# Kernel tuning notes

Hardware: AMD Instinct MI355X
Metric: run time of the kernel (lower is better)

## Reference

```python
import jax, jax.numpy as jnp
import numpy as np

LOG2E = 1.4426950408889634  # 1/ln(2): kernel works in log2 space with exp2


def _mlstm_chunkwise_single(q, k, v, vecI, vecF, chunk_size):
    # q,k: [T,K]; v: [T,V]; vecI,vecF: [T] (log2-space gate preactivations)
    T, K = q.shape
    V = v.shape[-1]
    BT = chunk_size
    NT = T // BT
    scale = K ** -0.5
    dt = q.dtype

    qc = q.reshape(NT, BT, K)
    kc = k.reshape(NT, BT, K)
    vc = v.reshape(NT, BT, V)
    ic = vecI.reshape(NT, BT)
    fc = vecF.reshape(NT, BT)
    b = jnp.cumsum(fc, axis=1)            # within-chunk cumulative log2 forget (vecF in kernel)
    f_last = b[:, -1]                      # scaF_last
    g = ic + f_last[:, None] - b           # decay from each pos to chunk end (vecG)

    tri = jnp.tril(jnp.ones((BT, BT), dtype=bool))

    def step(carry, inp):
        C, n, m = carry                    # [K,V], [K], scalar running max
        qt, kt, vt, it, bt, gt, fl = inp
        # intra-chunk decay matrix D[t,s] = i[s] + b[t] - b[s] for s<=t
        D = it[None, :] + bt[:, None] - bt[None, :]
        D = jnp.where(tri, D, -jnp.inf)
        m_intra = jnp.max(D, axis=1)                      # [BT]
        m_total = jnp.maximum(bt + m, m_intra)            # matM_total
        S = (qt @ kt.T) * (scale * jnp.exp2(D - m_total[:, None]))
        q_sc = qt * (scale * jnp.exp2(bt + m - m_total))[:, None]
        h_num = q_sc @ C + S @ vt                          # [BT,V]
        denom = jnp.maximum(jnp.abs(q_sc @ n + S.sum(axis=1)), jnp.exp2(-m_total))
        h = h_num / denom[:, None]
        # cross-chunk matrix-state recurrence with log2 restabilization
        m_next = jnp.maximum(fl + m, jnp.max(gt))
        dec = jnp.exp2(fl + m - m_next)
        kdec = kt * jnp.exp2(gt - m_next)[:, None]         # [BT,K]
        C_next = C * dec + kdec.T @ vt
        n_next = n * dec + kdec.sum(axis=0)
        return (C_next, n_next, m_next), h

    C0 = jnp.zeros((K, V), dt)
    n0 = jnp.zeros((K,), dt)
    m0 = jnp.zeros((), dt)
    _, hs = jax.lax.scan(step, (C0, n0, m0), (qc, kc, vc, ic, b, g, f_last))
    return hs.reshape(T, V)


def setup_inputs() -> dict:
    key = jax.random.key(0)
    ks = jax.random.split(key, 5)
    B, H, T, D = 8, 8, 4096, 64
    q = jax.random.normal(ks[0], (B, H, T, D), dtype=jnp.float32)
    k = jax.random.normal(ks[1], (B, H, T, D), dtype=jnp.float32)
    v = jax.random.normal(ks[2], (B, H, T, D), dtype=jnp.float32)
    i = jax.random.normal(ks[3], (B, H, T), dtype=jnp.float32)
    f = jax.random.normal(ks[4], (B, H, T), dtype=jnp.float32)
    return {"q": q, "k": k, "v": v, "i": i, "f": f, "chunk_size": 64}


def reference(q, k, v, i, f, chunk_size):
    B, H, T, K = q.shape
    V = v.shape[-1]
    vecF = jax.nn.log_sigmoid(f) * LOG2E   # log2 sigmoid(f)
    vecI = i * LOG2E                       # input gate in log2 space
    BH = B * H
    fn = lambda qq, kk, vv, ii, ff: _mlstm_chunkwise_single(qq, kk, vv, ii, ff, chunk_size)
    h = jax.vmap(fn)(q.reshape(BH, T, K), k.reshape(BH, T, K), v.reshape(BH, T, V),
                     vecI.reshape(BH, T), vecF.reshape(BH, T))
    return h.reshape(B, H, T, V)
```

## Files before the change

kernel.cpp:

```cpp
#include <hip/hip_runtime.h>
#include <hip/hip_bf16.h>
#include <math.h>

#define LOG2E_F 1.4426950408889634f

static constexpr int BT = 64;
static constexpr int DK = 64;
static constexpr int DV = 64;
static constexpr float SCALE = 0.125f;
static constexpr int PAD = 72;

typedef unsigned short ushort_t;
typedef __attribute__((ext_vector_type(8))) short short8;
typedef __attribute__((ext_vector_type(4))) float f32x4;
typedef __attribute__((ext_vector_type(4))) ushort_t ushort4v;

#define MFMA16(a, b, c) __builtin_amdgcn_mfma_f32_16x16x32_bf16((a), (b), (c), 0, 0, 0)

__device__ __forceinline__ int SWZ(int a, int b){ return a * PAD + (b ^ (((a >> 3) & 3) << 3)); }
__device__ __forceinline__ int ZSW(int r, int c){ return r * PAD + (c ^ (((r >> 2) & 3) << 3)); }
__device__ __forceinline__ int LIN(int r, int c){ return r * PAD + c; }

__device__ __forceinline__ float logsig_log2e(float x){
    float l = (x >= 0.f) ? (-log1pf(expf(-x))) : (x - log1pf(expf(x)));
    return l * LOG2E_F;
}
__device__ __forceinline__ ushort_t f2bf(float x){
    unsigned u = __builtin_bit_cast(unsigned, x);
    unsigned r = u + 0x7FFFu + ((u >> 16) & 1u);
    return (ushort_t)(r >> 16);
}
__device__ __forceinline__ float bf2f(ushort_t u){
    return __builtin_bit_cast(float, ((unsigned)u) << 16);
}
__device__ __forceinline__ void split_bf(float x, ushort_t& h, ushort_t& l){
    h = f2bf(x);
    l = f2bf(x - bf2f(h));
}

__global__ __launch_bounds__(256, 4) void stageA_kernel(
    const float* __restrict__ kg, const float* __restrict__ vg,
    const float* __restrict__ ig, const float* __restrict__ fg,
    float* __restrict__ A_ws, float* __restrict__ nloc_ws,
    float* __restrict__ fl_ws, float* __restrict__ mloc_ws,
    int T, int NT)
{
    const int ct = blockIdx.x, s = blockIdx.y, tid = threadIdx.x;
    const int w = tid >> 6, lane = tid & 63, ln = lane & 15, quad = lane >> 4;
    const int q8 = quad * 8;

    __shared__ __align__(16) ushort_t kth[BT * PAD];
    __shared__ __align__(16) ushort_t ktl[BT * PAD];
    __shared__ __align__(16) ushort_t vth[BT * PAD];
    __shared__ __align__(16) ushort_t vtl[BT * PAD];
    __shared__ float gsc[BT];

    const size_t rowbase = (size_t)s * T + (size_t)ct * BT;
    const float* kc = kg + rowbase * DK;
    const float* vc = vg + rowbase * DV;

    float4 kr[4], vr[4];
    #pragma unroll
    for (int i = 0; i < 4; ++i){
        int idx = i * 1024 + tid * 4;
        kr[i] = *(const float4*)(kc + idx);
        vr[i] = *(const float4*)(vc + idx);
    }
    if (tid < 64){
        float b = logsig_log2e(fg[rowbase + tid]);
        #pragma unroll
        for (int off = 1; off < 64; off <<= 1){
            float y = __shfl_up(b, off);
            if (tid >= off) b += y;
        }
        float f_last = __shfl(b, 63);
        float a = ig[rowbase + tid] * LOG2E_F - b;
        float p = a;
        #pragma unroll
        for (int off = 32; off > 0; off >>= 1) p = fmaxf(p, __shfl_xor(p, off));
        gsc[tid] = exp2f(a - p);
        if (tid == 0){ fl_ws[s * NT + ct] = f_last; mloc_ws[s * NT + ct] = f_last + p; }
    }
    __syncthreads();
    #pragma unroll
    for (int i = 0; i < 4; ++i){
        int idx = i * 1024 + tid * 4;
        int r = idx >> 6, c0 = idx & 63;
        float g = gsc[r];
        float kv[4] = {kr[i].x * g, kr[i].y * g, kr[i].z * g, kr[i].w * g};
        float vv[4] = {vr[i].x, vr[i].y, vr[i].z, vr[i].w};
        #pragma unroll
        for (int j = 0; j < 4; ++j){
            ushort_t h, l;
            split_bf(kv[j], h, l); kth[SWZ(c0 + j, r)] = h; ktl[SWZ(c0 + j, r)] = l;
            split_bf(vv[j], h, l); vth[SWZ(c0 + j, r)] = h; vtl[SWZ(c0 + j, r)] = l;
        }
    }
    __syncthreads();

    const int m = 16 * w + ln;
    short8 ah0 = *(const short8*)&kth[SWZ(m, q8)];
    short8 ah1 = *(const short8*)&kth[SWZ(m, 32 + q8)];
    short8 al0 = *(const short8*)&ktl[SWZ(m, q8)];
    short8 al1 = *(const short8*)&ktl[SWZ(m, 32 + q8)];
    float* Ab = A_ws + (size_t)(s * NT + ct) * 4096;
    #pragma unroll
    for (int t = 0; t < 4; ++t){
        f32x4 acc = {0.f, 0.f, 0.f, 0.f};
        short8 bh0 = *(const short8*)&vth[SWZ(16 * t + ln, q8)];
        short8 bh1 = *(const short8*)&vth[SWZ(16 * t + ln, 32 + q8)];
        short8 bl0 = *(const short8*)&vtl[SWZ(16 * t + ln, q8)];
        short8 bl1 = *(const short8*)&vtl[SWZ(16 * t + ln, 32 + q8)];
        acc = MFMA16(ah0, bh0, acc);
        acc = MFMA16(ah1, bh1, acc);
        acc = MFMA16(ah0, bl0, acc);
        acc = MFMA16(ah1, bl1, acc);
        acc = MFMA16(al0, bh0, acc);
        acc = MFMA16(al1, bh1, acc);
        *(f32x4*)(Ab + ((16 * t + ln) << 6) + 16 * w + quad * 4) = acc;
    }
    {
        short8 ones;
        #pragma unroll
        for (int j = 0; j < 8; ++j) ones[j] = (short)0x3F80;
        f32x4 nacc = {0.f, 0.f, 0.f, 0.f};
        nacc = MFMA16(ah0, ones, nacc);
        nacc = MFMA16(ah1, ones, nacc);
        nacc = MFMA16(al0, ones, nacc);
        nacc = MFMA16(al1, ones, nacc);
        if (ln == 0){
            #pragma unroll
            for (int reg = 0; reg < 4; ++reg)
                nloc_ws[((size_t)(s * NT + ct)) * DK + 16 * w + quad * 4 + reg] = nacc[reg];
        }
    }
}

__global__ __launch_bounds__(256) void stageB_kernel(
    const float* __restrict__ A_ws, const float* __restrict__ nloc_ws,
    const float* __restrict__ fl_ws, const float* __restrict__ mloc_ws,
    float* __restrict__ Cws, float* __restrict__ nws, float* __restrict__ mws,
    int NT)
{
    const int vb = blockIdx.x, s = blockIdx.y, tid = threadIdx.x;
    __shared__ float decs[64], scs[64];

    if (tid < 64){
        float fl = fl_ws[s * NT + tid];
        float ml = mloc_ws[s * NT + tid];
        float F = fl, G = ml;
        #pragma unroll
        for (int off = 1; off < 64; off <<= 1){
            float Fp = __shfl_up(F, off);
            float Gp = __shfl_up(G, off);
            if (tid >= off){ G = fmaxf(Gp + F, G); F = Fp + F; }
        }
        float m_next = fmaxf(F, G);
        float m_cur  = __shfl_up(m_next, 1);
        if (tid == 0) m_cur = 0.f;
        decs[tid] = exp2f(fl + m_cur - m_next);
        scs[tid]  = exp2f(ml - m_next);
        if (vb == 0) mws[s * NT + tid] = m_cur;
    }
    __syncthreads();

    const size_t base = (size_t)s * NT * 4096 + (size_t)vb * 256 + tid;
    const float* Ab = A_ws + base;
    float*       Cb = Cws  + base;
    const bool do_n = (vb == 0) && (tid < 64);

    float C = 0.f, nreg = 0.f;
    float p[8], nl[8];
    #pragma unroll
    for (int i = 0; i < 8; ++i){ p[i] = Ab[(size_t)i * 4096]; nl[i] = 0.f; }
    if (do_n){
        #pragma unroll
        for (int i = 0; i < 8; ++i) nl[i] = nloc_ws[((size_t)(s * NT + i)) * DK + tid];
    }

    for (int t0 = 0; t0 < NT; t0 += 8){
        float qv[8], nq[8];
        const int tn = t0 + 8;
        #pragma unroll
        for (int i = 0; i < 8; ++i)
            qv[i] = (tn + i < NT) ? Ab[(size_t)(tn + i) * 4096] : 0.f;
        #pragma unroll
        for (int i = 0; i < 8; ++i) nq[i] = 0.f;
        if (do_n){
            #pragma unroll
            for (int i = 0; i < 8; ++i)
                if (tn + i < NT) nq[i] = nloc_ws[((size_t)(s * NT + tn + i)) * DK + tid];
        }
        #pragma unroll
        for (int i = 0; i < 8; ++i){
            const int t = t0 + i;
            Cb[(size_t)t * 4096] = C;
            if (do_n) nws[((size_t)(s * NT + t)) * DK + tid] = nreg;
            const float d = decs[t], sc = scs[t];
            C = C * d + p[i] * sc;
            if (do_n) nreg = nreg * d + nl[i] * sc;
        }
        #pragma unroll
        for (int i = 0; i < 8; ++i){ p[i] = qv[i]; nl[i] = nq[i]; }
    }
}

__global__ __launch_bounds__(256, 4) void pass2_kernel(
    const float* __restrict__ qg, const float* __restrict__ kg, const float* __restrict__ vg,
    const float* __restrict__ ig, const float* __restrict__ fg,
    const float* __restrict__ Cws, const float* __restrict__ nws, const float* __restrict__ mws,
    float* __restrict__ out, int T, int NT)
{
    const int ct = blockIdx.x, s = blockIdx.y, tid = threadIdx.x;
    const int w = tid >> 6, lane = tid & 63, ln = lane & 15, quad = lane >> 4;
    const int q8 = quad * 8;

    __shared__ __align__(16) ushort_t bufA[BT * PAD];
    __shared__ __align__(16) ushort_t bufB[BT * PAD];
    __shared__ __align__(16) ushort_t bufZ[BT * PAD];
    __shared__ __align__(16) ushort_t bufV[BT * PAD];
    __shared__ float colterm[BT], Mr[BT], rowfac[BT], dncl[BT];
    __shared__ float nsh[DK], qn[BT], rowsum[BT];

    const size_t rowbase = (size_t)s * T + (size_t)ct * BT;
    const float* qc = qg + rowbase * DK;
    const float* kc = kg + rowbase * DK;
    const float* vc = vg + rowbase * DV;
    const float* Cc = Cws + ((size_t)(s * NT + ct)) * 4096;
    const float* nc = nws + ((size_t)(s * NT + ct)) * DK;
    const float m   = mws[s * NT + ct];

    float4 kr4[4], vr[4];
    #pragma unroll
    for (int i = 0; i < 4; ++i){
        int idx = i * 1024 + tid * 4;
        kr4[i] = *(const float4*)(kc + idx);
        vr[i]  = *(const float4*)(vc + idx);
    }
    const float* qrow = qc + (16 * w + ln) * DK;
    float4 qf0 = *(const float4*)(qrow + q8);
    float4 qf1 = *(const float4*)(qrow + q8 + 4);
    float4 qf2 = *(const float4*)(qrow + 32 + q8);
    float4 qf3 = *(const float4*)(qrow + 32 + q8 + 4);
    float4 Cr[4];
    #pragma unroll
    for (int i = 0; i < 4; ++i)
        Cr[i] = *(const float4*)(Cc + i * 1024 + tid * 4);

    if (tid < 64){
        float b = logsig_log2e(fg[rowbase + tid]);
        #pragma unroll
        for (int off = 1; off < 64; off <<= 1){
            float y = __shfl_up(b, off);
            if (tid >= off) b += y;
        }
        float a = ig[rowbase + tid] * LOG2E_F - b;
        float p = a;
        #pragma unroll
        for (int off = 1; off < 64; off <<= 1){
            float y = __shfl_up(p, off);
            if (tid >= off) p = fmaxf(p, y);
        }
        float M = fmaxf(m, p);
        colterm[tid] = a;
        Mr[tid] = M;
        rowfac[tid] = SCALE * exp2f(m - M);
        dncl[tid] = exp2f(-(b + M));
        nsh[tid] = nc[tid];
    }
    #pragma unroll
    for (int i = 0; i < 4; ++i){
        int idx = i * 1024 + tid * 4;
        int r = idx >> 6, c0 = idx & 63;
        float kv[4] = {kr4[i].x, kr4[i].y, kr4[i].z, kr4[i].w};
        ushort4v kh4, kl4;
        #pragma unroll
        for (int j = 0; j < 4; ++j){
            ushort_t h, l;
            split_bf(kv[j], h, l); kh4[j] = h; kl4[j] = l;
        }
        *(ushort4v*)&bufA[SWZ(r, c0)] = kh4;
        *(ushort4v*)&bufB[SWZ(r, c0)] = kl4;
    }
    __syncthreads();

    const int mrow = 16 * w + ln;
    float a0[8] = {qf0.x, qf0.y, qf0.z, qf0.w, qf1.x, qf1.y, qf1.z, qf1.w};
    float a1[8] = {qf2.x, qf2.y, qf2.z, qf2.w, qf3.x, qf3.y, qf3.z, qf3.w};
    short8 ah0, al0, ah1, al1;
    #pragma unroll
    for (int j = 0; j < 8; ++j){
        ushort_t h, l;
        split_bf(a0[j], h, l); ah0[j] = (short)h; al0[j] = (short)l;
        split_bf(a1[j], h, l); ah1[j] = (short)h; al1[j] = (short)l;
    }
    {
        float p = 0.f;
        #pragma unroll
        for (int j = 0; j < 8; ++j){
            p = fmaf(a0[j], nsh[q8 + j], p);
            p = fmaf(a1[j], nsh[32 + q8 + j], p);
        }
        p += __shfl_xor(p, 16);
        p += __shfl_xor(p, 32);
        if (quad == 0) qn[mrow] = p;
    }
    #pragma unroll
    for (int i = 0; i < 4; ++i){
        int idx = i * 1024 + tid * 4;
        int r = idx >> 6, c0 = idx & 63;
        float vv[4] = {vr[i].x, vr[i].y, vr[i].z, vr[i].w};
        #pragma unroll
        for (int j = 0; j < 4; ++j) bufV[SWZ(c0 + j, r)] = f2bf(vv[j]);
    }

    f32x4 sacc[4];
    #pragma unroll
    for (int t = 0; t < 4; ++t){
        sacc[t] = (f32x4){0.f, 0.f, 0.f, 0.f};
        short8 bh0 = *(const short8*)&bufA[SWZ(16 * t + ln, q8)];
        short8 bh1 = *(const short8*)&bufA[SWZ(16 * t + ln, 32 + q8)];
        short8 bl0 = *(const short8*)&bufB[SWZ(16 * t + ln, q8)];
        short8 bl1 = *(const short8*)&bufB[SWZ(16 * t + ln, 32 + q8)];
        sacc[t] = MFMA16(ah0, bh0, sacc[t]);
        sacc[t] = MFMA16(ah1, bh1, sacc[t]);
        sacc[t] = MFMA16(ah0, bl0, sacc[t]);
        sacc[t] = MFMA16(ah1, bl1, sacc[t]);
        sacc[t] = MFMA16(al0, bh0, sacc[t]);
        sacc[t] = MFMA16(al1, bh1, sacc[t]);
    }
    {
        float rsum[4] = {0.f, 0.f, 0.f, 0.f};
        float Mrv[4];
        #pragma unroll
        for (int reg = 0; reg < 4; ++reg) Mrv[reg] = Mr[16 * w + quad * 4 + reg];
        #pragma unroll
        for (int t = 0; t < 4; ++t){
            int c = 16 * t + ln;
            float cterm = colterm[c];
            #pragma unroll
            for (int reg = 0; reg < 4; ++reg){
                int r = 16 * w + quad * 4 + reg;
                float vS = (c <= r) ? sacc[t][reg] * SCALE * exp2f(cterm - Mrv[reg]) : 0.f;
                bufZ[ZSW(r, c)] = f2bf(vS);
                rsum[reg] += vS;
            }
        }
        #pragma unroll
        for (int off = 1; off < 16; off <<= 1){
            #pragma unroll
            for (int reg = 0; reg < 4; ++reg) rsum[reg] += __shfl_xor(rsum[reg], off);
        }
        if (ln == 0){
            #pragma unroll
            for (int reg = 0; reg < 4; ++reg) rowsum[16 * w + quad * 4 + reg] = rsum[reg];
        }
    }
    __syncthreads();

    #pragma unroll
    for (int i = 0; i < 4; ++i){
        int idx = i * 1024 + tid * 4;
        int vrow = idx >> 6, k0 = idx & 63;
        float cv[4] = {Cr[i].x, Cr[i].y, Cr[i].z, Cr[i].w};
        ushort4v ch4, cl4;
        #pragma unroll
        for (int j = 0; j < 4; ++j){
            ushort_t h, l;
            split_bf(cv[j], h, l); ch4[j] = h; cl4[j] = l;
        }
        *(ushort4v*)&bufA[SWZ(vrow, k0)] = ch4;
        *(ushort4v*)&bufB[SWZ(vrow, k0)] = cl4;
    }
    __syncthreads();

    f32x4 acc[4];
    #pragma unroll
    for (int t = 0; t < 4; ++t){
        acc[t] = (f32x4){0.f, 0.f, 0.f, 0.f};
        short8 bh0 = *(const short8*)&bufA[SWZ(16 * t + ln, q8)];
        short8 bh1 = *(const short8*)&bufA[SWZ(16 * t + ln, 32 + q8)];
        short8 bl0 = *(const short8*)&bufB[SWZ(16 * t + ln, q8)];
        short8 bl1 = *(const short8*)&bufB[SWZ(16 * t + ln, 32 + q8)];
        acc[t] = MFMA16(ah0, bh0, acc[t]);
        acc[t] = MFMA16(ah1, bh1, acc[t]);
        acc[t] = MFMA16(ah0, bl0, acc[t]);
        acc[t] = MFMA16(ah1, bl1, acc[t]);
        acc[t] = MFMA16(al0, bh0, acc[t]);
        acc[t] = MFMA16(al1, bh1, acc[t]);
    }
    float rf[4], inv[4];
    #pragma unroll
    for (int reg = 0; reg < 4; ++reg){
        int r = 16 * w + quad * 4 + reg;
        rf[reg] = rowfac[r];
        float dn = fabsf(rf[reg] * qn[r] + rowsum[r]);
        inv[reg] = 1.f / fmaxf(dn, dncl[r]);
    }
    #pragma unroll
    for (int t = 0; t < 4; ++t){
        #pragma unroll
        for (int reg = 0; reg < 4; ++reg) acc[t][reg] *= rf[reg];
    }
    short8 az0 = *(const short8*)&bufZ[ZSW(mrow, q8)];
    short8 az1 = *(const short8*)&bufZ[ZSW(mrow, 32 + q8)];
    #pragma unroll
    for (int t = 0; t < 4; ++t){
        short8 bh0 = *(const short8*)&bufV[SWZ(16 * t + ln, q8)];
        short8 bh1 = *(const short8*)&bufV[SWZ(16 * t + ln, 32 + q8)];
        acc[t] = MFMA16(az0, bh0, acc[t]);
        acc[t] = MFMA16(az1, bh1, acc[t]);
    }
    #pragma unroll
    for (int t = 0; t < 4; ++t){
        int c = 16 * t + ln;
        #pragma unroll
        for (int reg = 0; reg < 4; ++reg){
            int r = 16 * w + quad * 4 + reg;
            out[(rowbase + r) * DV + c] = acc[t][reg] * inv[reg];
        }
    }
}

__global__ __launch_bounds__(256) void fused_kernel(
    const float* __restrict__ qg, const float* __restrict__ kg, const float* __restrict__ vg,
    const float* __restrict__ ig, const float* __restrict__ fg,
    float* __restrict__ out, int T, int NT)
{
    const int s = blockIdx.x;
    const int tid = threadIdx.x;
    const int lane = tid & 63;

    __shared__ float X[BT][DK + 1];
    __shared__ float Y[BT][DK + 1];
    __shared__ float Cb[DK][DV];
    __shared__ __hip_bfloat16 Zh[BT][BT];
    __shared__ float colterm[BT], Mr[BT], rowfac[BT], dncl[BT], gscale[BT];
    __shared__ float nsh[DK], qn[BT], rowsum[BT], denom[BT];
    __shared__ float sh_dec;

    const float* qseq = qg + (size_t)s * T * DK;
    const float* kseq = kg + (size_t)s * T * DK;
    const float* vseq = vg + (size_t)s * T * DV;
    const float* iseq = ig + (size_t)s * T;
    const float* fseq = fg + (size_t)s * T;

    for (int idx = tid; idx < DK * DV; idx += 256) Cb[idx >> 6][idx & 63] = 0.f;
    if (tid < 64) nsh[lane] = 0.f;
    float m = 0.f;
    __syncthreads();

    const int r0 = (tid >> 4) * 4;
    const int c0 = (tid & 15) * 4;
    const int v0 = c0;

    for (int t = 0; t < NT; ++t){
        const size_t rb = (size_t)t * BT;
        if (tid < 64){
            float b = logsig_log2e(fseq[rb + lane]);
            #pragma unroll
            for (int off = 1; off < 64; off <<= 1){
                float y = __shfl_up(b, off);
                if (lane >= off) b += y;
            }
            float f_last = __shfl(b, 63);
            float a = iseq[rb + lane] * LOG2E_F - b;
            float p = a;
            #pragma unroll
            for (int off = 1; off < 64; off <<= 1){
                float y = __shfl_up(p, off);
                if (lane >= off) p = fmaxf(p, y);
            }
            float M = fmaxf(m, p);
            colterm[lane] = a;
            Mr[lane] = M;
            rowfac[lane] = SCALE * exp2f(m - M);
            dncl[lane] = exp2f(-(b + M));
            float g = a + f_last;
            float gm = g;
            #pragma unroll
            for (int off = 32; off > 0; off >>= 1) gm = fmaxf(gm, __shfl_xor(gm, off));
            float m_next = fmaxf(f_last + m, gm);
            gscale[lane] = exp2f(g - m_next);
            if (tid == 0) sh_dec = exp2f(f_last + m - m_next);
            m = m_next;
        }
        #pragma unroll
        for (int base = 0; base < BT * DK; base += 1024){
            int idx = base + tid * 4;
            int r = idx >> 6, c = idx & 63;
            float4 a4 = *(const float4*)(qseq + rb * DK + idx);
            X[r][c] = a4.x; X[r][c+1] = a4.y; X[r][c+2] = a4.z; X[r][c+3] = a4.w;
            float4 b4 = *(const float4*)(kseq + rb * DK + idx);
            Y[r][c] = b4.x; Y[r][c+1] = b4.y; Y[r][c+2] = b4.z; Y[r][c+3] = b4.w;
        }
        __syncthreads();

        float sacc[4][4] = {};
        for (int x = 0; x < DK; ++x){
            float xr[4], yc[4];
            #pragma unroll
            for (int j = 0; j < 4; ++j) xr[j] = X[r0 + j][x];
            #pragma unroll
            for (int j = 0; j < 4; ++j) yc[j] = Y[c0 + j][x];
            #pragma unroll
            for (int j = 0; j < 4; ++j)
                #pragma unroll
                for (int jj = 0; jj < 4; ++jj)
                    sacc[j][jj] = fmaf(xr[j], yc[jj], sacc[j][jj]);
        }
        float rs[4];
        #pragma unroll
        for (int j = 0; j < 4; ++j){
            int r = r0 + j;
            float Mrv = Mr[r];
            float acc = 0.f;
            #pragma unroll
            for (int jj = 0; jj < 4; ++jj){
                int c = c0 + jj;
                float vS = (c <= r) ? sacc[j][jj] * SCALE * exp2f(colterm[c] - Mrv) : 0.f;
                Zh[r][c] = __float2bfloat16(vS);
                acc += vS;
            }
            rs[j] = acc;
        }
        #pragma unroll
        for (int off = 1; off < 16; off <<= 1){
            #pragma unroll
            for (int j = 0; j < 4; ++j) rs[j] += __shfl_xor(rs[j], off);
        }
        if ((tid & 15) == 0){
            #pragma unroll
            for (int j = 0; j < 4; ++j) rowsum[r0 + j] = rs[j];
        }
        float acc1[4][4] = {};
        for (int x = 0; x < DK; ++x){
            float xr[4], yv[4];
            #pragma unroll
            for (int j = 0; j < 4; ++j) xr[j] = X[r0 + j][x];
            #pragma unroll
            for (int j = 0; j < 4; ++j) yv[j] = Cb[x][v0 + j];
            #pragma unroll
            for (int j = 0; j < 4; ++j)
                #pragma unroll
                for (int jj = 0; jj < 4; ++jj)
                    acc1[j][jj] = fmaf(xr[j], yv[jj], acc1[j][jj]);
        }
        if (tid < 64){
            float acc = 0.f;
            for (int x = 0; x < DK; ++x) acc = fmaf(X[lane][x], nsh[x], acc);
            qn[lane] = acc;
        }
        __syncthreads();

        #pragma unroll
        for (int base = 0; base < BT * DV; base += 1024){
            int idx = base + tid * 4;
            int r = idx >> 6, c = idx & 63;
            float4 a4 = *(const float4*)(vseq + rb * DV + idx);
            X[r][c] = a4.x; X[r][c+1] = a4.y; X[r][c+2] = a4.z; X[r][c+3] = a4.w;
        }
        if (tid < 64){
            float dn = fabsf(rowfac[lane] * qn[lane] + rowsum[lane]);
            denom[lane] = fmaxf(dn, dncl[lane]);
        }
        __syncthreads();

        float acc2[4][4] = {};
        for (int c = 0; c < BT; ++c){
            float zr[4], xv[4];
            #pragma unroll
            for (int j = 0; j < 4; ++j) zr[j] = __bfloat162float(Zh[r0 + j][c]);
            #pragma unroll
            for (int j = 0; j < 4; ++j) xv[j] = X[c][v0 + j];
            #pragma unroll
            for (int j = 0; j < 4; ++j)
                #pragma unroll
                for (int jj = 0; jj < 4; ++jj)
                    acc2[j][jj] = fmaf(zr[j], xv[jj], acc2[j][jj]);
        }
        #pragma unroll
        for (int j = 0; j < 4; ++j){
            int r = r0 + j;
            float rf = rowfac[r];
            float inv = 1.f / denom[r];
            float4 h4;
            h4.x = (acc1[j][0] * rf + acc2[j][0]) * inv;
            h4.y = (acc1[j][1] * rf + acc2[j][1]) * inv;
            h4.z = (acc1[j][2] * rf + acc2[j][2]) * inv;
            h4.w = (acc1[j][3] * rf + acc2[j][3]) * inv;
            *(float4*)(out + ((size_t)s * T + rb + r) * DV + v0) = h4;
        }
        {
            float dec = sh_dec;
            float cr[4][4];
            #pragma unroll
            for (int j = 0; j < 4; ++j)
                #pragma unroll
                for (int jj = 0; jj < 4; ++jj)
                    cr[j][jj] = Cb[r0 + j][c0 + jj] * dec;
            for (int c = 0; c < BT; ++c){
                float gs = gscale[c];
                float kd[4], xv[4];
                #pragma unroll
                for (int j = 0; j < 4; ++j) kd[j] = Y[c][r0 + j] * gs;
                #pragma unroll
                for (int jj = 0; jj < 4; ++jj) xv[jj] = X[c][c0 + jj];
                #pragma unroll
                for (int j = 0; j < 4; ++j)
                    #pragma unroll
                    for (int jj = 0; jj < 4; ++jj)
                        cr[j][jj] = fmaf(kd[j], xv[jj], cr[j][jj]);
            }
            #pragma unroll
            for (int j = 0; j < 4; ++j)
                #pragma unroll
                for (int jj = 0; jj < 4; ++jj)
                    Cb[r0 + j][c0 + jj] = cr[j][jj];
        }
        if (tid < 64){
            float acc = 0.f;
            for (int c = 0; c < BT; ++c) acc = fmaf(Y[c][lane], gscale[c], acc);
            nsh[lane] = nsh[lane] * sh_dec + acc;
        }
        __syncthreads();
    }
}

extern "C" void kernel_launch(void* const* d_in, const int* in_sizes, int n_in,
                              void* d_out, int out_size, void* d_ws, size_t ws_size,
                              hipStream_t stream)
{
    const float* q  = (const float*)d_in[0];
    const float* k  = (const float*)d_in[1];
    const float* v  = (const float*)d_in[2];
    const float* ii = (const float*)d_in[3];
    const float* ff = (const float*)d_in[4];
    float* out = (float*)d_out;

    const int T  = 4096;
    const int BH = in_sizes[3] / T;
    const int NT = T / BT;

    const size_t szC  = (size_t)BH * NT * DK * DV * sizeof(float);
    const size_t szA  = szC;
    const size_t szn  = (size_t)BH * NT * DK * sizeof(float);
    const size_t szs  = (size_t)BH * NT * sizeof(float);

    const size_t need_new = szA + szC + 2 * szn + 3 * szs;

    if (ws_size >= need_new){
        char* p = (char*)d_ws;
        float* A_ws    = (float*)p;            p += szA;
        float* Cws     = (float*)p;            p += szC;
        float* nloc_ws = (float*)p;            p += szn;
        float* nws     = (float*)p;            p += szn;
        float* fl_ws   = (float*)p;            p += szs;
        float* mloc_ws = (float*)p;            p += szs;
        float* mws     = (float*)p;
        stageA_kernel<<<dim3(NT, BH), 256, 0, stream>>>(k, v, ii, ff, A_ws, nloc_ws, fl_ws, mloc_ws, T, NT);
        stageB_kernel<<<dim3(16, BH), 256, 0, stream>>>(A_ws, nloc_ws, fl_ws, mloc_ws, Cws, nws, mws, NT);
        pass2_kernel<<<dim3(NT, BH), 256, 0, stream>>>(q, k, v, ii, ff, Cws, nws, mws, out, T, NT);
    } else {
        fused_kernel<<<dim3(BH), 256, 0, stream>>>(q, k, v, ii, ff, out, T, NT);
    }
}
```

Measured before the change: 292.1 us.

## Checkpoint chunk states every four chunks and recompute intermediates in pass2

StageB now writes the inter-chunk C/n state only at every fourth chunk, plus per-chunk decay and scale factors. Pass2 processes four consecutive chunks per block and rebuilds the running state in registers from the checkpoint and the per-chunk A contributions. This cuts the write and re-read of the full per-chunk C state workspace. In exchange it reads A_ws again, launches four times fewer pass2 blocks with a serial loop inside each, and recombines q from its split bf16 halves, which slightly changes rounding.

```diff
diff --git a/kernel.cpp b/kernel.cpp
--- a/kernel.cpp
+++ b/kernel.cpp
@@ -9,6 +9,7 @@
 static constexpr int DV = 64;
 static constexpr float SCALE = 0.125f;
 static constexpr int PAD = 72;
+static constexpr int CPB = 4;
 
 typedef unsigned short ushort_t;
 typedef __attribute__((ext_vector_type(8))) short short8;
@@ -19,7 +20,6 @@
 
 __device__ __forceinline__ int SWZ(int a, int b){ return a * PAD + (b ^ (((a >> 3) & 3) << 3)); }
 __device__ __forceinline__ int ZSW(int r, int c){ return r * PAD + (c ^ (((r >> 2) & 3) << 3)); }
-__device__ __forceinline__ int LIN(int r, int c){ return r * PAD + c; }
 
 __device__ __forceinline__ float logsig_log2e(float x){
     float l = (x >= 0.f) ? (-log1pf(expf(-x))) : (x - log1pf(expf(x)));
@@ -139,10 +139,12 @@
 __global__ __launch_bounds__(256) void stageB_kernel(
     const float* __restrict__ A_ws, const float* __restrict__ nloc_ws,
     const float* __restrict__ fl_ws, const float* __restrict__ mloc_ws,
-    float* __restrict__ Cws, float* __restrict__ nws, float* __restrict__ mws,
+    float* __restrict__ Cb_ws, float* __restrict__ nb_ws,
+    float* __restrict__ mws, float* __restrict__ decs_ws, float* __restrict__ scs_ws,
     int NT)
 {
     const int vb = blockIdx.x, s = blockIdx.y, tid = threadIdx.x;
+    const int NG = NT >> 2;
     __shared__ float decs[64], scs[64];
 
     if (tid < 64){
@@ -158,15 +160,20 @@
         float m_next = fmaxf(F, G);
         float m_cur  = __shfl_up(m_next, 1);
         if (tid == 0) m_cur = 0.f;
-        decs[tid] = exp2f(fl + m_cur - m_next);
-        scs[tid]  = exp2f(ml - m_next);
-        if (vb == 0) mws[s * NT + tid] = m_cur;
+        float d  = exp2f(fl + m_cur - m_next);
+        float sc = exp2f(ml - m_next);
+        decs[tid] = d;
+        scs[tid]  = sc;
+        if (vb == 0){
+            mws[s * NT + tid]     = m_cur;
+            decs_ws[s * NT + tid] = d;
+            scs_ws[s * NT + tid]  = sc;
+        }
     }
     __syncthreads();
 
     const size_t base = (size_t)s * NT * 4096 + (size_t)vb * 256 + tid;
     const float* Ab = A_ws + base;
-    float*       Cb = Cws  + base;
     const bool do_n = (vb == 0) && (tid < 64);
 
     float C = 0.f, nreg = 0.f;
@@ -194,8 +201,11 @@
         #pragma unroll
         for (int i = 0; i < 8; ++i){
             const int t = t0 + i;
-            Cb[(size_t)t * 4096] = C;
-            if (do_n) nws[((size_t)(s * NT + t)) * DK + tid] = nreg;
+            if ((t & 3) == 0){
+                const int g = t >> 2;
+                Cb_ws[((size_t)(s * NG + g)) * 4096 + (size_t)vb * 256 + tid] = C;
+                if (do_n) nb_ws[((size_t)(s * NG + g)) * 64 + tid] = nreg;
+            }
             const float d = decs[t], sc = scs[t];
             C = C * d + p[i] * sc;
             if (do_n) nreg = nreg * d + nl[i] * sc;
@@ -208,12 +218,17 @@
 __global__ __launch_bounds__(256, 4) void pass2_kernel(
     const float* __restrict__ qg, const float* __restrict__ kg, const float* __restrict__ vg,
     const float* __restrict__ ig, const float* __restrict__ fg,
-    const float* __restrict__ Cws, const float* __restrict__ nws, const float* __restrict__ mws,
+    const float* __restrict__ A_ws, const float* __restrict__ Cb_ws,
+    const float* __restrict__ nb_ws, const float* __restrict__ nloc_ws,
+    const float* __restrict__ mws, const float* __restrict__ decs_ws,
+    const float* __restrict__ scs_ws,
     float* __restrict__ out, int T, int NT)
 {
-    const int ct = blockIdx.x, s = blockIdx.y, tid = threadIdx.x;
+    const int g = blockIdx.x, s = blockIdx.y, tid = threadIdx.x;
     const int w = tid >> 6, lane = tid & 63, ln = lane & 15, quad = lane >> 4;
     const int q8 = quad * 8;
+    const int ct0 = g * CPB;
+    const int NG = NT >> 2;
 
     __shared__ __align__(16) ushort_t bufA[BT * PAD];
     __shared__ __align__(16) ushort_t bufB[BT * PAD];
@@ -222,203 +237,239 @@
     __shared__ float colterm[BT], Mr[BT], rowfac[BT], dncl[BT];
     __shared__ float nsh[DK], qn[BT], rowsum[BT];
 
-    const size_t rowbase = (size_t)s * T + (size_t)ct * BT;
-    const float* qc = qg + rowbase * DK;
-    const float* kc = kg + rowbase * DK;
-    const float* vc = vg + rowbase * DV;
-    const float* Cc = Cws + ((size_t)(s * NT + ct)) * 4096;
-    const float* nc = nws + ((size_t)(s * NT + ct)) * DK;
-    const float m   = mws[s * NT + ct];
-
-    float4 kr4[4], vr[4];
+    f32x4 Crun[4];
+    {
+        const float* Cb = Cb_ws + ((size_t)(s * NG + g)) * 4096;
+        #pragma unroll
+        for (int i = 0; i < 4; ++i)
+            Crun[i] = *(const f32x4*)(Cb + i * 1024 + tid * 4);
+    }
+    if (tid < 64) nsh[tid] = nb_ws[((size_t)(s * NG + g)) * 64 + tid];
+
+    float fvs[CPB], ivs[CPB], nlv[CPB], mvs[CPB], dcv[CPB], scv[CPB];
     #pragma unroll
-    for (int i = 0; i < 4; ++i){
-        int idx = i * 1024 + tid * 4;
-        kr4[i] = *(const float4*)(kc + idx);
-        vr[i]  = *(const float4*)(vc + idx);
-    }
-    const float* qrow = qc + (16 * w + ln) * DK;
-    float4 qf0 = *(const float4*)(qrow + q8);
-    float4 qf1 = *(const float4*)(qrow + q8 + 4);
-    float4 qf2 = *(const float4*)(qrow + 32 + q8);
-    float4 qf3 = *(const float4*)(qrow + 32 + q8 + 4);
-    float4 Cr[4];
+    for (int c = 0; c < CPB; ++c){
+        const int ct = ct0 + c;
+        const size_t rb = (size_t)s * T + (size_t)ct * BT;
+        fvs[c] = 0.f; ivs[c] = 0.f; nlv[c] = 0.f;
+        if (tid < 64){
+            fvs[c] = fg[rb + tid];
+            ivs[c] = ig[rb + tid];
+            nlv[c] = nloc_ws[((size_t)(s * NT + ct)) * DK + tid];
+        }
+        mvs[c] = mws[s * NT + ct];
+        dcv[c] = decs_ws[s * NT + ct];
+        scv[c] = scs_ws[s * NT + ct];
+    }
+
     #pragma unroll
-    for (int i = 0; i < 4; ++i)
-        Cr[i] = *(const float4*)(Cc + i * 1024 + tid * 4);
-
-    if (tid < 64){
-        float b = logsig_log2e(fg[rowbase + tid]);
-        #pragma unroll
-        for (int off = 1; off < 64; off <<= 1){
-            float y = __shfl_up(b, off);
-            if (tid >= off) b += y;
-        }
-        float a = ig[rowbase + tid] * LOG2E_F - b;
-        float p = a;
-        #pragma unroll
-        for (int off = 1; off < 64; off <<= 1){
-            float y = __shfl_up(p, off);
-            if (tid >= off) p = fmaxf(p, y);
-        }
-        float M = fmaxf(m, p);
-        colterm[tid] = a;
-        Mr[tid] = M;
-        rowfac[tid] = SCALE * exp2f(m - M);
-        dncl[tid] = exp2f(-(b + M));
-        nsh[tid] = nc[tid];
-    }
-    #pragma unroll
-    for (int i = 0; i < 4; ++i){
-        int idx = i * 1024 + tid * 4;
-        int r = idx >> 6, c0 = idx & 63;
-        float kv[4] = {kr4[i].x, kr4[i].y, kr4[i].z, kr4[i].w};
-        ushort4v kh4, kl4;
-        #pragma unroll
-        for (int j = 0; j < 4; ++j){
-            ushort_t h, l;
-            split_bf(kv[j], h, l); kh4[j] = h; kl4[j] = l;
-        }
-        *(ushort4v*)&bufA[SWZ(r, c0)] = kh4;
-        *(ushort4v*)&bufB[SWZ(r, c0)] = kl4;
-    }
-    __syncthreads();
-
-    const int mrow = 16 * w + ln;
-    float a0[8] = {qf0.x, qf0.y, qf0.z, qf0.w, qf1.x, qf1.y, qf1.z, qf1.w};
-    float a1[8] = {qf2.x, qf2.y, qf2.z, qf2.w, qf3.x, qf3.y, qf3.z, qf3.w};
-    short8 ah0, al0, ah1, al1;
-    #pragma unroll
-    for (int j = 0; j < 8; ++j){
-        ushort_t h, l;
-        split_bf(a0[j], h, l); ah0[j] = (short)h; al0[j] = (short)l;
-        split_bf(a1[j], h, l); ah1[j] = (short)h; al1[j] = (short)l;
-    }
-    {
-        float p = 0.f;
-        #pragma unroll
-        for (int j = 0; j < 8; ++j){
-            p = fmaf(a0[j], nsh[q8 + j], p);
-            p = fmaf(a1[j], nsh[32 + q8 + j], p);
-        }
-        p += __shfl_xor(p, 16);
-        p += __shfl_xor(p, 32);
-        if (quad == 0) qn[mrow] = p;
-    }
-    #pragma unroll
-    for (int i = 0; i < 4; ++i){
-        int idx = i * 1024 + tid * 4;
-        int r = idx >> 6, c0 = idx & 63;
-        float vv[4] = {vr[i].x, vr[i].y, vr[i].z, vr[i].w};
-        #pragma unroll
-        for (int j = 0; j < 4; ++j) bufV[SWZ(c0 + j, r)] = f2bf(vv[j]);
-    }
-
-    f32x4 sacc[4];
-    #pragma unroll
-    for (int t = 0; t < 4; ++t){
-        sacc[t] = (f32x4){0.f, 0.f, 0.f, 0.f};
-        short8 bh0 = *(const short8*)&bufA[SWZ(16 * t + ln, q8)];
-        short8 bh1 = *(const short8*)&bufA[SWZ(16 * t + ln, 32 + q8)];
-        short8 bl0 = *(const short8*)&bufB[SWZ(16 * t + ln, q8)];
-        short8 bl1 = *(const short8*)&bufB[SWZ(16 * t + ln, 32 + q8)];
-        sacc[t] = MFMA16(ah0, bh0, sacc[t]);
-        sacc[t] = MFMA16(ah1, bh1, sacc[t]);
-        sacc[t] = MFMA16(ah0, bl0, sacc[t]);
-        sacc[t] = MFMA16(ah1, bl1, sacc[t]);
-        sacc[t] = MFMA16(al0, bh0, sacc[t]);
-        sacc[t] = MFMA16(al1, bh1, sacc[t]);
-    }
-    {
-        float rsum[4] = {0.f, 0.f, 0.f, 0.f};
-        float Mrv[4];
-        #pragma unroll
-        for (int reg = 0; reg < 4; ++reg) Mrv[reg] = Mr[16 * w + quad * 4 + reg];
+    for (int c = 0; c < CPB; ++c){
+        const int ct = ct0 + c;
+        const size_t rowbase = (size_t)s * T + (size_t)ct * BT;
+
+        float4 kr4[4], vr[4], qf[4];
+        #pragma unroll
+        for (int i = 0; i < 4; ++i){
+            int idx = i * 1024 + tid * 4;
+            kr4[i] = *(const float4*)(kg + rowbase * DK + idx);
+            vr[i]  = *(const float4*)(vg + rowbase * DV + idx);
+        }
+        {
+            const float* qrow = qg + (rowbase + 16 * w + ln) * DK;
+            qf[0] = *(const float4*)(qrow + q8);
+            qf[1] = *(const float4*)(qrow + q8 + 4);
+            qf[2] = *(const float4*)(qrow + 32 + q8);
+            qf[3] = *(const float4*)(qrow + 32 + q8 + 4);
+        }
+        if (tid < 64){
+            float b = logsig_log2e(fvs[c]);
+            #pragma unroll
+            for (int off = 1; off < 64; off <<= 1){
+                float y = __shfl_up(b, off);
+                if (tid >= off) b += y;
+            }
+            float a = ivs[c] * LOG2E_F - b;
+            float p = a;
+            #pragma unroll
+            for (int off = 1; off < 64; off <<= 1){
+                float y = __shfl_up(p, off);
+                if (tid >= off) p = fmaxf(p, y);
+            }
+            float M = fmaxf(mvs[c], p);
+            colterm[tid] = a;
+            Mr[tid] = M;
+            rowfac[tid] = SCALE * exp2f(mvs[c] - M);
+            dncl[tid] = exp2f(-(b + M));
+        }
+        #pragma unroll
+        for (int i = 0; i < 4; ++i){
+            int idx = i * 1024 + tid * 4;
+            int r = idx >> 6, c0 = idx & 63;
+            float kv[4] = {kr4[i].x, kr4[i].y, kr4[i].z, kr4[i].w};
+            ushort4v kh4, kl4;
+            #pragma unroll
+            for (int j = 0; j < 4; ++j){
+                ushort_t h, l;
+                split_bf(kv[j], h, l); kh4[j] = h; kl4[j] = l;
+            }
+            *(ushort4v*)&bufA[SWZ(r, c0)] = kh4;
+            *(ushort4v*)&bufB[SWZ(r, c0)] = kl4;
+        }
+        short8 ah0, al0, ah1, al1;
+        {
+            float a0t[8] = {qf[0].x, qf[0].y, qf[0].z, qf[0].w, qf[1].x, qf[1].y, qf[1].z, qf[1].w};
+            float a1t[8] = {qf[2].x, qf[2].y, qf[2].z, qf[2].w, qf[3].x, qf[3].y, qf[3].z, qf[3].w};
+            #pragma unroll
+            for (int j = 0; j < 8; ++j){
+                ushort_t h, l;
+                split_bf(a0t[j], h, l); ah0[j] = (short)h; al0[j] = (short)l;
+                split_bf(a1t[j], h, l); ah1[j] = (short)h; al1[j] = (short)l;
+            }
+        }
+        f32x4 Ar[4];
+        if (c + 1 < CPB){
+            const float* Ab = A_ws + ((size_t)(s * NT + ct)) * 4096;
+            #pragma unroll
+            for (int i = 0; i < 4; ++i)
+                Ar[i] = *(const f32x4*)(Ab + i * 1024 + tid * 4);
+        }
+        __syncthreads();
+
+        const int mrow = 16 * w + ln;
+        {
+            float p = 0.f;
+            #pragma unroll
+            for (int j = 0; j < 8; ++j){
+                float qv0 = bf2f((ushort_t)ah0[j]) + bf2f((ushort_t)al0[j]);
+                float qv1 = bf2f((ushort_t)ah1[j]) + bf2f((ushort_t)al1[j]);
+                p = fmaf(qv0, nsh[q8 + j], p);
+                p = fmaf(qv1, nsh[32 + q8 + j], p);
+            }
+            p += __shfl_xor(p, 16);
+            p += __shfl_xor(p, 32);
+            if (quad == 0) qn[mrow] = p;
+        }
+        #pragma unroll
+        for (int i = 0; i < 4; ++i){
+            int idx = i * 1024 + tid * 4;
+            int r = idx >> 6, c0 = idx & 63;
+            float vv[4] = {vr[i].x, vr[i].y, vr[i].z, vr[i].w};
+            #pragma unroll
+            for (int j = 0; j < 4; ++j) bufV[SWZ(c0 + j, r)] = f2bf(vv[j]);
+        }
+        f32x4 sacc[4];
         #pragma unroll
         for (int t = 0; t < 4; ++t){
-            int c = 16 * t + ln;
-            float cterm = colterm[c];
+            sacc[t] = (f32x4){0.f, 0.f, 0.f, 0.f};
+            short8 bh0 = *(const short8*)&bufA[SWZ(16 * t + ln, q8)];
+            short8 bh1 = *(const short8*)&bufA[SWZ(16 * t + ln, 32 + q8)];
+            short8 bl0 = *(const short8*)&bufB[SWZ(16 * t + ln, q8)];
+            short8 bl1 = *(const short8*)&bufB[SWZ(16 * t + ln, 32 + q8)];
+            sacc[t] = MFMA16(ah0, bh0, sacc[t]);
+            sacc[t] = MFMA16(ah1, bh1, sacc[t]);
+            sacc[t] = MFMA16(ah0, bl0, sacc[t]);
+            sacc[t] = MFMA16(ah1, bl1, sacc[t]);
+            sacc[t] = MFMA16(al0, bh0, sacc[t]);
+            sacc[t] = MFMA16(al1, bh1, sacc[t]);
+        }
+        {
+            float rsum[4] = {0.f, 0.f, 0.f, 0.f};
+            float Mrv[4];
+            #pragma unroll
+            for (int reg = 0; reg < 4; ++reg) Mrv[reg] = Mr[16 * w + quad * 4 + reg];
+            #pragma unroll
+            for (int t = 0; t < 4; ++t){
+                int cc = 16 * t + ln;
+                float cterm = colterm[cc];
+                #pragma unroll
+                for (int reg = 0; reg < 4; ++reg){
+                    int r = 16 * w + quad * 4 + reg;
+                    float vS = (cc <= r) ? sacc[t][reg] * SCALE * exp2f(cterm - Mrv[reg]) : 0.f;
+                    bufZ[ZSW(r, cc)] = f2bf(vS);
+                    rsum[reg] += vS;
+                }
+            }
+            #pragma unroll
+            for (int off = 1; off < 16; off <<= 1){
+                #pragma unroll
+                for (int reg = 0; reg < 4; ++reg) rsum[reg] += __shfl_xor(rsum[reg], off);
+            }
+            if (ln == 0){
+                #pragma unroll
+                for (int reg = 0; reg < 4; ++reg) rowsum[16 * w + quad * 4 + reg] = rsum[reg];
+            }
+        }
+        __syncthreads();
+
+        #pragma unroll
+        for (int i = 0; i < 4; ++i){
+            int idx = i * 1024 + tid * 4;
+            int vrow = idx >> 6, k0 = idx & 63;
+            float cv[4] = {Crun[i][0], Crun[i][1], Crun[i][2], Crun[i][3]};
+            ushort4v ch4, cl4;
+            #pragma unroll
+            for (int j = 0; j < 4; ++j){
+                ushort_t h, l;
+                split_bf(cv[j], h, l); ch4[j] = h; cl4[j] = l;
+            }
+            *(ushort4v*)&bufA[SWZ(vrow, k0)] = ch4;
+            *(ushort4v*)&bufB[SWZ(vrow, k0)] = cl4;
+        }
+        if (c + 1 < CPB){
+            #pragma unroll
+            for (int i = 0; i < 4; ++i)
+                Crun[i] = Crun[i] * dcv[c] + Ar[i] * scv[c];
+            if (tid < 64) nsh[tid] = nsh[tid] * dcv[c] + nlv[c] * scv[c];
+        }
+        __syncthreads();
+
+        f32x4 acc[4];
+        #pragma unroll
+        for (int t = 0; t < 4; ++t){
+            acc[t] = (f32x4){0.f, 0.f, 0.f, 0.f};
+            short8 bh0 = *(const short8*)&bufA[SWZ(16 * t + ln, q8)];
+            short8 bh1 = *(const short8*)&bufA[SWZ(16 * t + ln, 32 + q8)];
+            short8 bl0 = *(const short8*)&bufB[SWZ(16 * t + ln, q8)];
+            short8 bl1 = *(const short8*)&bufB[SWZ(16 * t + ln, 32 + q8)];
+            acc[t] = MFMA16(ah0, bh0, acc[t]);
+            acc[t] = MFMA16(ah1, bh1, acc[t]);
+            acc[t] = MFMA16(ah0, bl0, acc[t]);
+            acc[t] = MFMA16(ah1, bl1, acc[t]);
+            acc[t] = MFMA16(al0, bh0, acc[t]);
+            acc[t] = MFMA16(al1, bh1, acc[t]);
+        }
+        float rf[4], inv[4];
+        #pragma unroll
+        for (int reg = 0; reg < 4; ++reg){
+            int r = 16 * w + quad * 4 + reg;
+            rf[reg] = rowfac[r];
+            float dn = fabsf(rf[reg] * qn[r] + rowsum[r]);
+            inv[reg] = 1.f / fmaxf(dn, dncl[r]);
+        }
+        #pragma unroll
+        for (int t = 0; t < 4; ++t){
+            #pragma unroll
+            for (int reg = 0; reg < 4; ++reg) acc[t][reg] *= rf[reg];
+        }
+        short8 az0 = *(const short8*)&bufZ[ZSW(mrow, q8)];
+        short8 az1 = *(const short8*)&bufZ[ZSW(mrow, 32 + q8)];
+        #pragma unroll
+        for (int t = 0; t < 4; ++t){
+            short8 bh0 = *(const short8*)&bufV[SWZ(16 * t + ln, q8)];
+            short8 bh1 = *(const short8*)&bufV[SWZ(16 * t + ln, 32 + q8)];
+            acc[t] = MFMA16(az0, bh0, acc[t]);
+            acc[t] = MFMA16(az1, bh1, acc[t]);
+        }
+        #pragma unroll
+        for (int t = 0; t < 4; ++t){
+            int cc = 16 * t + ln;
             #pragma unroll
             for (int reg = 0; reg < 4; ++reg){
                 int r = 16 * w + quad * 4 + reg;
-                float vS = (c <= r) ? sacc[t][reg] * SCALE * exp2f(cterm - Mrv[reg]) : 0.f;
-                bufZ[ZSW(r, c)] = f2bf(vS);
-                rsum[reg] += vS;
-            }
-        }
-        #pragma unroll
-        for (int off = 1; off < 16; off <<= 1){
-            #pragma unroll
-            for (int reg = 0; reg < 4; ++reg) rsum[reg] += __shfl_xor(rsum[reg], off);
-        }
-        if (ln == 0){
-            #pragma unroll
-            for (int reg = 0; reg < 4; ++reg) rowsum[16 * w + quad * 4 + reg] = rsum[reg];
-        }
-    }
-    __syncthreads();
-
-    #pragma unroll
-    for (int i = 0; i < 4; ++i){
-        int idx = i * 1024 + tid * 4;
-        int vrow = idx >> 6, k0 = idx & 63;
-        float cv[4] = {Cr[i].x, Cr[i].y, Cr[i].z, Cr[i].w};
-        ushort4v ch4, cl4;
-        #pragma unroll
-        for (int j = 0; j < 4; ++j){
-            ushort_t h, l;
-            split_bf(cv[j], h, l); ch4[j] = h; cl4[j] = l;
-        }
-        *(ushort4v*)&bufA[SWZ(vrow, k0)] = ch4;
-        *(ushort4v*)&bufB[SWZ(vrow, k0)] = cl4;
-    }
-    __syncthreads();
-
-    f32x4 acc[4];
-    #pragma unroll
-    for (int t = 0; t < 4; ++t){
-        acc[t] = (f32x4){0.f, 0.f, 0.f, 0.f};
-        short8 bh0 = *(const short8*)&bufA[SWZ(16 * t + ln, q8)];
-        short8 bh1 = *(const short8*)&bufA[SWZ(16 * t + ln, 32 + q8)];
-        short8 bl0 = *(const short8*)&bufB[SWZ(16 * t + ln, q8)];
-        short8 bl1 = *(const short8*)&bufB[SWZ(16 * t + ln, 32 + q8)];
-        acc[t] = MFMA16(ah0, bh0, acc[t]);
-        acc[t] = MFMA16(ah1, bh1, acc[t]);
-        acc[t] = MFMA16(ah0, bl0, acc[t]);
-        acc[t] = MFMA16(ah1, bl1, acc[t]);
-        acc[t] = MFMA16(al0, bh0, acc[t]);
-        acc[t] = MFMA16(al1, bh1, acc[t]);
-    }
-    float rf[4], inv[4];
-    #pragma unroll
-    for (int reg = 0; reg < 4; ++reg){
-        int r = 16 * w + quad * 4 + reg;
-        rf[reg] = rowfac[r];
-        float dn = fabsf(rf[reg] * qn[r] + rowsum[r]);
-        inv[reg] = 1.f / fmaxf(dn, dncl[r]);
-    }
-    #pragma unroll
-    for (int t = 0; t < 4; ++t){
-        #pragma unroll
-        for (int reg = 0; reg < 4; ++reg) acc[t][reg] *= rf[reg];
-    }
-    short8 az0 = *(const short8*)&bufZ[ZSW(mrow, q8)];
-    short8 az1 = *(const short8*)&bufZ[ZSW(mrow, 32 + q8)];
-    #pragma unroll
-    for (int t = 0; t < 4; ++t){
-        short8 bh0 = *(const short8*)&bufV[SWZ(16 * t + ln, q8)];
-        short8 bh1 = *(const short8*)&bufV[SWZ(16 * t + ln, 32 + q8)];
-        acc[t] = MFMA16(az0, bh0, acc[t]);
-        acc[t] = MFMA16(az1, bh1, acc[t]);
-    }
-    #pragma unroll
-    for (int t = 0; t < 4; ++t){
-        int c = 16 * t + ln;
-        #pragma unroll
-        for (int reg = 0; reg < 4; ++reg){
-            int r = 16 * w + quad * 4 + reg;
-            out[(rowbase + r) * DV + c] = acc[t][reg] * inv[reg];
-        }
+                out[(rowbase + r) * DV + cc] = acc[t][reg] * inv[reg];
+            }
+        }
+        if (c + 1 < CPB) __syncthreads();
     }
 }
 
@@ -641,26 +692,30 @@
     const int T  = 4096;
     const int BH = in_sizes[3] / T;
     const int NT = T / BT;
-
-    const size_t szC  = (size_t)BH * NT * DK * DV * sizeof(float);
-    const size_t szA  = szC;
-    const size_t szn  = (size_t)BH * NT * DK * sizeof(float);
-    const size_t szs  = (size_t)BH * NT * sizeof(float);
-
-    const size_t need_new = szA + szC + 2 * szn + 3 * szs;
-
-    if (ws_size >= need_new){
+    const int NG = NT / CPB;
+
+    const size_t szA   = (size_t)BH * NT * DK * DV * sizeof(float);
+    const size_t szCb  = (size_t)BH * NG * DK * DV * sizeof(float);
+    const size_t szn   = (size_t)BH * NT * DK * sizeof(float);
+    const size_t sznb  = (size_t)BH * NG * DK * sizeof(float);
+    const size_t szs   = (size_t)BH * NT * sizeof(float);
+
+    const size_t need_new = szA + szCb + szn + sznb + 5 * szs;
+
+    if (ws_size >= need_new && NT == 64){
         char* p = (char*)d_ws;
         float* A_ws    = (float*)p;            p += szA;
-        float* Cws     = (float*)p;            p += szC;
+        float* Cb_ws   = (float*)p;            p += szCb;
         float* nloc_ws = (float*)p;            p += szn;
-        float* nws     = (float*)p;            p += szn;
+        float* nb_ws   = (float*)p;            p += sznb;
         float* fl_ws   = (float*)p;            p += szs;
         float* mloc_ws = (float*)p;            p += szs;
-        float* mws     = (float*)p;
+        float* mws     = (float*)p;            p += szs;
+        float* decs_ws = (float*)p;            p += szs;
+        float* scs_ws  = (float*)p;
         stageA_kernel<<<dim3(NT, BH), 256, 0, stream>>>(k, v, ii, ff, A_ws, nloc_ws, fl_ws, mloc_ws, T, NT);
-        stageB_kernel<<<dim3(16, BH), 256, 0, stream>>>(A_ws, nloc_ws, fl_ws, mloc_ws, Cws, nws, mws, NT);
-        pass2_kernel<<<dim3(NT, BH), 256, 0, stream>>>(q, k, v, ii, ff, Cws, nws, mws, out, T, NT);
+        stageB_kernel<<<dim3(16, BH), 256, 0, stream>>>(A_ws, nloc_ws, fl_ws, mloc_ws, Cb_ws, nb_ws, mws, decs_ws, scs_ws, NT);
+        pass2_kernel<<<dim3(NG, BH), 256, 0, stream>>>(q, k, v, ii, ff, A_ws, Cb_ws, nb_ws, nloc_ws, mws, decs_ws, scs_ws, out, T, NT);
     } else {
         fused_kernel<<<dim3(BH), 256, 0, stream>>>(q, k, v, ii, ff, out, T, NT);
     }
```

New measurement: 369.1 us. 26.3% more time.
